# Optimization experiments

Hardware: AMD Instinct MI355X
Metric: run time of the kernel (lower is better)

## Reference

```python
import jax, jax.numpy as jnp
import numpy as np

MARGIN = 0.2
EPS = 1e-6  # torch.pairwise_distance default eps added to (x1 - x2)


def setup_inputs() -> dict:
    key = jax.random.key(0)
    k1, k2 = jax.random.split(key)
    N, D = 8192, 128
    x = jax.random.normal(k1, (N, D), dtype=jnp.float32)
    target = jax.random.randint(k2, (N,), 0, 1000)
    return {"x": x, "target": target}


def _pairwise_dist(x):
    # torch.pairwise_distance(x.unsqueeze(0), x.unsqueeze(1)):
    #   diff[i, j] = x[j] - x[i] + EPS ; dist[i, j] = ||diff[i, j]||_2
    # Expanded quadratic form avoids the [N, N, D] diff tensor:
    #   ||a - b + e||^2 = ||a||^2 + ||b||^2 - 2 a.b + 2e*sum(a - b) + D*e^2
    sq = jnp.sum(x * x, axis=1)          # [N]
    s = jnp.sum(x, axis=1)               # [N]
    dot = x @ x.T                        # [N, N]
    D = x.shape[1]
    d2 = (sq[None, :] + sq[:, None] - 2.0 * dot
          + 2.0 * EPS * (s[None, :] - s[:, None]) + D * EPS * EPS)
    return jnp.sqrt(jnp.maximum(d2, 0.0))


def reference(x, target):
    N = x.shape[0]
    dist = _pairwise_dist(x)                                 # [N, N]
    same = target[None, :] == target[:, None]                # [N, N] bool
    pos_mask = (same & ~jnp.eye(N, dtype=bool)).astype(x.dtype)
    hardest_pos = jnp.max(pos_mask * dist, axis=1, keepdims=True)  # [N, 1]
    neg_mask = (~same).astype(x.dtype)
    max_neg = jnp.max(dist, axis=1, keepdims=True)           # [N, 1]
    anchor_neg = dist + max_neg * (1.0 - neg_mask)           # push positives up
    hardest_neg = jnp.min(anchor_neg, axis=1, keepdims=True) # [N, 1]
    loss = jax.nn.relu(hardest_pos - hardest_neg + MARGIN)
    return jnp.mean(loss)
```

## Files before the change

### kernel.cpp

```cpp
#include <hip/hip_runtime.h>

#define N 8192
#define Dk 128
#define NC 1024
#define EPSC 1e-6f
#define MARGIN 0.2f

typedef __attribute__((ext_vector_type(8))) short bf16x8;
typedef __attribute__((ext_vector_type(4))) float f32x4;

__device__ __forceinline__ unsigned short f2bf(float f) {
    unsigned u = __float_as_uint(f);
    u = (u + 0x7FFFu + ((u >> 16) & 1u)) >> 16;
    return (unsigned short)u;
}

__global__ void hist_kernel(const int* __restrict__ tgt, int* __restrict__ hist) {
    int i = blockIdx.x * 256 + threadIdx.x;
    atomicAdd(&hist[tgt[i]], 1);
}

__global__ void scan_kernel(const int* __restrict__ hist, int* __restrict__ pref,
                            int* __restrict__ cursor) {
    __shared__ int tmp[NC];
    int t = threadIdx.x;
    int h = hist[t];
    tmp[t] = h;
    __syncthreads();
#pragma unroll
    for (int off = 1; off < NC; off <<= 1) {
        int v = (t >= off) ? tmp[t - off] : 0;
        __syncthreads();
        tmp[t] += v;
        __syncthreads();
    }
    int ex = tmp[t] - h;
    pref[t] = ex;
    cursor[t] = ex;
}

__global__ void scatter_kernel(const int* __restrict__ tgt, const int* __restrict__ pref,
                               const int* __restrict__ hist, int* __restrict__ cursor,
                               int* __restrict__ perm, uint2* __restrict__ band,
                               int* __restrict__ cls) {
    int i = blockIdx.x * 256 + threadIdx.x;
    int c = tgt[i];
    int pos = atomicAdd(&cursor[c], 1);
    perm[pos] = i;
    uint2 b;
    b.x = (unsigned)pref[c];
    b.y = (unsigned)(pref[c] + hist[c]);
    band[pos] = b;
    cls[pos] = c;
}

__global__ void prep_kernel(const float* __restrict__ x, const int* __restrict__ perm,
                            uint4* __restrict__ Frag, float* __restrict__ Qh,
                            float* __restrict__ P) {
    int wv = blockIdx.x * 4 + (threadIdx.x >> 6);
    int lane = threadIdx.x & 63;
    int k = wv * 4 + (lane >> 4);
    int c = lane & 15;
    int orig = perm[k];
    const float4* x4 = reinterpret_cast<const float4*>(x);
    float4 v0 = x4[orig * 32 + c * 2];
    float4 v1 = x4[orig * 32 + c * 2 + 1];
    float sq = v0.x * v0.x + v0.y * v0.y + v0.z * v0.z + v0.w * v0.w +
               v1.x * v1.x + v1.y * v1.y + v1.z * v1.z + v1.w * v1.w;
    float s = v0.x + v0.y + v0.z + v0.w + v1.x + v1.y + v1.z + v1.w;
    ushort4 lo, hi;
    lo.x = f2bf(v0.x); lo.y = f2bf(v0.y); lo.z = f2bf(v0.z); lo.w = f2bf(v0.w);
    hi.x = f2bf(v1.x); hi.y = f2bf(v1.y); hi.z = f2bf(v1.z); hi.w = f2bf(v1.w);
    uint4 pk;
    pk.x = (unsigned)lo.x | ((unsigned)lo.y << 16);
    pk.y = (unsigned)lo.z | ((unsigned)lo.w << 16);
    pk.z = (unsigned)hi.x | ((unsigned)hi.y << 16);
    pk.w = (unsigned)hi.z | ((unsigned)hi.w << 16);
    Frag[((k >> 4) * 4 + (c >> 2)) * 64 + (c & 3) * 16 + (k & 15)] = pk;
#pragma unroll
    for (int m = 1; m <= 8; m <<= 1) {
        sq += __shfl_xor(sq, m);
        s += __shfl_xor(s, m);
    }
    if (c == 0) {
        P[k] = sq - 2.0f * EPSC * s;
        Qh[k] = -0.5f * (sq + 2.0f * EPSC * s + (float)Dk * EPSC * EPSC);
    }
}

#define LOADB(Bb, Qq, t)                                                \
    do {                                                                \
        const int jt_ = jt0 + (t);                                      \
        Bb[0] = Fr[(jt_ * 4 + 0) * 64 + lane];                          \
        Bb[1] = Fr[(jt_ * 4 + 1) * 64 + lane];                          \
        Bb[2] = Fr[(jt_ * 4 + 2) * 64 + lane];                          \
        Bb[3] = Fr[(jt_ * 4 + 3) * 64 + lane];                          \
        Qq = *reinterpret_cast<const f32x4*>(&Qh[jt_ * 16 + 4 * q]);    \
    } while (0)

#define MFMA16(ACC, Bb, Qq)                                                           \
    do {                                                                              \
        _Pragma("unroll")                                                             \
        for (int ti = 0; ti < 4; ++ti) {                                              \
            ACC[ti] = __builtin_amdgcn_mfma_f32_16x16x32_bf16(Bb[0], Af[ti][0], Qq, 0, 0, 0); \
            ACC[ti] = __builtin_amdgcn_mfma_f32_16x16x32_bf16(Bb[1], Af[ti][1], ACC[ti], 0, 0, 0); \
            ACC[ti] = __builtin_amdgcn_mfma_f32_16x16x32_bf16(Bb[2], Af[ti][2], ACC[ti], 0, 0, 0); \
            ACC[ti] = __builtin_amdgcn_mfma_f32_16x16x32_bf16(Bb[3], Af[ti][3], ACC[ti], 0, 0, 0); \
        }                                                                             \
    } while (0)

#define EPILOGUE(ACC, t)                                                              \
    do {                                                                              \
        const int jc_ = (jt0 + (t)) * 16;                                             \
        if (jc_ < bHi && jc_ + 16 > bLo) {     \
            int4 cj = *reinterpret_cast<const int4*>(&cls[jc_ + 4 * q]);              \
            _Pragma("unroll")                                                         \
            for (int ti = 0; ti < 4; ++ti) {                                          \
                f32x4 v = ACC[ti];                                                    \
                int mc = myc[ti];                                                     \
                hp[ti] = fminf(hp[ti], cj.x == mc ? v[0] : INFINITY);                 \
                hp[ti] = fminf(hp[ti], cj.y == mc ? v[1] : INFINITY);                 \
                hp[ti] = fminf(hp[ti], cj.z == mc ? v[2] : INFINITY);                 \
                hp[ti] = fminf(hp[ti], cj.w == mc ? v[3] : INFINITY);                 \
                mn[ti] = fmaxf(mn[ti], cj.x == mc ? -INFINITY : v[0]);                \
                mn[ti] = fmaxf(mn[ti], cj.y == mc ? -INFINITY : v[1]);                \
                mn[ti] = fmaxf(mn[ti], cj.z == mc ? -INFINITY : v[2]);                \
                mn[ti] = fmaxf(mn[ti], cj.w == mc ? -INFINITY : v[3]);                \
            }                                                                         \
        } else {                \
            _Pragma("unroll")                                                         \
            for (int ti = 0; ti < 4; ++ti) {                                          \
                f32x4 v = ACC[ti];                                                    \
                mn[ti] = fmaxf(mn[ti], fmaxf(fmaxf(v[0], v[1]), fmaxf(v[2], v[3])));  \
            }                                                                         \
        }                                                                             \
    } while (0)

#define STEP(t, ACCc, ACCp, Bc, Qc, Bp, Qp)   \
    do {                                      \
        MFMA16(ACCc, Bc, Qc);                 \
        if ((t) + 2 < 16) LOADB(Bp, Qp, (t) + 2); \
        if ((t) > 0) EPILOGUE(ACCp, (t) - 1); \
    } while (0)

__global__ __launch_bounds__(256, 2) void main_kernel(
        const uint4* __restrict__ Frag, const float* __restrict__ Qh,
        const int* __restrict__ cls, const uint2* __restrict__ band,
        float* __restrict__ partHp, float* __restrict__ partMn) {
    const int w = threadIdx.x >> 6;
    const int lane = threadIdx.x & 63;
    const int n = lane & 15;
    const int q = lane >> 4;

    const int ig = (int)blockIdx.x >> 5;
    const int jg = (int)blockIdx.x & 31;
    const int rw = ig * 256 + 64 * w;
    const int jt0 = jg * 16;

    const bf16x8* Fr = reinterpret_cast<const bf16x8*>(Frag);

    const int bLo = (int)band[rw].x;
    const int bHi = (int)band[rw + 63].y;

    bf16x8 Af[4][4];
#pragma unroll
    for (int ti = 0; ti < 4; ++ti)
#pragma unroll
        for (int kk = 0; kk < 4; ++kk)
            Af[ti][kk] = Fr[(((rw >> 4) + ti) * 4 + kk) * 64 + lane];

    int myc[4];
#pragma unroll
    for (int ti = 0; ti < 4; ++ti) myc[ti] = cls[rw + 16 * ti + n];

    float hp[4], mn[4];
#pragma unroll
    for (int s = 0; s < 4; ++s) {
        hp[s] = INFINITY;
        mn[s] = -INFINITY;
    }

    bf16x8 B0[4], B1[4], B2[4];
    f32x4 Q0, Q1, Q2;
    f32x4 accA[4], accB[4];

    LOADB(B0, Q0, 0);
    LOADB(B1, Q1, 1);
    STEP(0, accA, accB, B0, Q0, B2, Q2);
    STEP(1, accB, accA, B1, Q1, B0, Q0);
    STEP(2, accA, accB, B2, Q2, B1, Q1);
    STEP(3, accB, accA, B0, Q0, B2, Q2);
    STEP(4, accA, accB, B1, Q1, B0, Q0);
    STEP(5, accB, accA, B2, Q2, B1, Q1);
    STEP(6, accA, accB, B0, Q0, B2, Q2);
    STEP(7, accB, accA, B1, Q1, B0, Q0);
    STEP(8, accA, accB, B2, Q2, B1, Q1);
    STEP(9, accB, accA, B0, Q0, B2, Q2);
    STEP(10, accA, accB, B1, Q1, B0, Q0);
    STEP(11, accB, accA, B2, Q2, B1, Q1);
    STEP(12, accA, accB, B0, Q0, B2, Q2);
    STEP(13, accB, accA, B1, Q1, B0, Q0);
    STEP(14, accA, accB, B2, Q2, B1, Q1);
    STEP(15, accB, accA, B0, Q0, B2, Q2);
    EPILOGUE(accB, 15);

#pragma unroll
    for (int m = 16; m <= 32; m <<= 1) {
#pragma unroll
        for (int s = 0; s < 4; ++s) {
            hp[s] = fminf(hp[s], __shfl_xor(hp[s], m));
            mn[s] = fmaxf(mn[s], __shfl_xor(mn[s], m));
        }
    }
    if (q == 0) {
#pragma unroll
        for (int ti = 0; ti < 4; ++ti) {
            int i = rw + 16 * ti + n;
            partHp[jg * N + i] = hp[ti];
            partMn[jg * N + i] = mn[ti];
        }
    }
}

__global__ void finish_kernel(const float* __restrict__ P,
                              const float* __restrict__ partHp,
                              const float* __restrict__ partMn,
                              float* __restrict__ out) {
    int i = blockIdx.x * 256 + threadIdx.x;
    float hpm = INFINITY, mnm = -INFINITY;
#pragma unroll
    for (int wg = 0; wg < 32; ++wg) {
        hpm = fminf(hpm, partHp[wg * N + i]);
        mnm = fmaxf(mnm, partMn[wg * N + i]);
    }
    float Pi = P[i];
    float hp = sqrtf(fmaxf(fmaf(-2.0f, hpm, Pi), 0.0f));
    float hn = sqrtf(fmaxf(fmaf(-2.0f, mnm, Pi), 0.0f));
    float sum = fmaxf(hp - hn + MARGIN, 0.0f) * (1.0f / (float)N);
#pragma unroll
    for (int m = 32; m >= 1; m >>= 1) sum += __shfl_xor(sum, m);
    __shared__ float ws[4];
    int lane = threadIdx.x & 63, wv = threadIdx.x >> 6;
    if (lane == 0) ws[wv] = sum;
    __syncthreads();
    if (threadIdx.x == 0) atomicAdd(out, ws[0] + ws[1] + ws[2] + ws[3]);
}

extern "C" void kernel_launch(void* const* d_in, const int* in_sizes, int n_in,
                              void* d_out, int out_size, void* d_ws, size_t ws_size,
                              hipStream_t stream) {
    const float* x = (const float*)d_in[0];
    const int* tgt = (const int*)d_in[1];
    float* out = (float*)d_out;

    char* ws = (char*)d_ws;
    size_t off = 0;
    uint4* Frag = (uint4*)(ws + off); off += (size_t)N * Dk * 2;
    float* Qh = (float*)(ws + off); off += (size_t)N * 4;
    float* P = (float*)(ws + off); off += (size_t)N * 4;
    float* partHp = (float*)(ws + off); off += (size_t)32 * N * 4;
    float* partMn = (float*)(ws + off); off += (size_t)32 * N * 4;
    uint2* band = (uint2*)(ws + off); off += (size_t)N * 8;
    int* perm = (int*)(ws + off); off += (size_t)N * 4;
    int* cls = (int*)(ws + off); off += (size_t)N * 4;
    int* hist = (int*)(ws + off); off += NC * 4;
    int* pref = (int*)(ws + off); off += NC * 4;
    int* cursor = (int*)(ws + off); off += NC * 4;

    hipMemsetAsync(hist, 0, NC * 4, stream);
    hipMemsetAsync(d_out, 0, sizeof(float), stream);
    hist_kernel<<<N / 256, 256, 0, stream>>>(tgt, hist);
    scan_kernel<<<1, NC, 0, stream>>>(hist, pref, cursor);
    scatter_kernel<<<N / 256, 256, 0, stream>>>(tgt, pref, hist, cursor, perm, band, cls);
    prep_kernel<<<N / 16, 256, 0, stream>>>(x, perm, Frag, Qh, P);
    main_kernel<<<1024, 256, 0, stream>>>(Frag, Qh, cls, band, partHp, partMn);
    finish_kernel<<<32, 256, 0, stream>>>(P, partHp, partMn, out);
}
```

Measured before the change: 102.7 us.

## Switch to 32x32x16 MFMA tiles and fuse label sort into one kernel

The main distance kernel moves from 16x16x32 bf16 MFMAs to 32x32x16 MFMAs, with a new 32-row fragment layout, per-tile packed Q and class arrays, and a two-deep double-buffered loop. Each block now covers a wider column range, so there are fewer column groups (8 instead of 32) and a smaller partial reduction in finish. The histogram, scan and scatter kernels plus both memsets are merged into one single-block shared-memory sort kernel, and a small qpack kernel is added that also zeroes the output. The aim is fewer launches and denser MFMA work per wave, at the cost of fewer blocks (512) and a larger register footprint.

Result: slower. 110.4 us (+7.5%).

```diff
diff --git a/kernel.cpp b/kernel.cpp
--- a/kernel.cpp
+++ b/kernel.cpp
@@ -7,7 +7,7 @@
 #define MARGIN 0.2f
 
 typedef __attribute__((ext_vector_type(8))) short bf16x8;
-typedef __attribute__((ext_vector_type(4))) float f32x4;
+typedef __attribute__((ext_vector_type(16))) float f32x16;
 
 __device__ __forceinline__ unsigned short f2bf(float f) {
     unsigned u = __float_as_uint(f);
@@ -15,43 +15,45 @@
     return (unsigned short)u;
 }
 
-__global__ void hist_kernel(const int* __restrict__ tgt, int* __restrict__ hist) {
-    int i = blockIdx.x * 256 + threadIdx.x;
-    atomicAdd(&hist[tgt[i]], 1);
-}
-
-__global__ void scan_kernel(const int* __restrict__ hist, int* __restrict__ pref,
-                            int* __restrict__ cursor) {
-    __shared__ int tmp[NC];
+__global__ void sort_kernel(const int* __restrict__ tgt, int* __restrict__ perm,
+                            int* __restrict__ cls, uint2* __restrict__ band) {
+    __shared__ int histS[NC], prefS[NC], curS[NC];
     int t = threadIdx.x;
-    int h = hist[t];
-    tmp[t] = h;
-    __syncthreads();
-#pragma unroll
+    histS[t] = 0;
+    __syncthreads();
+    int myt[8];
+#pragma unroll
+    for (int k = 0; k < 8; ++k) {
+        myt[k] = tgt[k * 1024 + t];
+        atomicAdd(&histS[myt[k]], 1);
+    }
+    __syncthreads();
+    int h = histS[t];
+    prefS[t] = h;
+    __syncthreads();
     for (int off = 1; off < NC; off <<= 1) {
-        int v = (t >= off) ? tmp[t - off] : 0;
+        int v = (t >= off) ? prefS[t - off] : 0;
         __syncthreads();
-        tmp[t] += v;
+        prefS[t] += v;
         __syncthreads();
     }
-    int ex = tmp[t] - h;
-    pref[t] = ex;
-    cursor[t] = ex;
-}
-
-__global__ void scatter_kernel(const int* __restrict__ tgt, const int* __restrict__ pref,
-                               const int* __restrict__ hist, int* __restrict__ cursor,
-                               int* __restrict__ perm, uint2* __restrict__ band,
-                               int* __restrict__ cls) {
-    int i = blockIdx.x * 256 + threadIdx.x;
-    int c = tgt[i];
-    int pos = atomicAdd(&cursor[c], 1);
-    perm[pos] = i;
-    uint2 b;
-    b.x = (unsigned)pref[c];
-    b.y = (unsigned)(pref[c] + hist[c]);
-    band[pos] = b;
-    cls[pos] = c;
+    int ex = prefS[t] - h;
+    __syncthreads();
+    prefS[t] = ex;
+    curS[t] = ex;
+    __syncthreads();
+#pragma unroll
+    for (int k = 0; k < 8; ++k) {
+        int i = k * 1024 + t;
+        int c = myt[k];
+        int pos = atomicAdd(&curS[c], 1);
+        perm[pos] = i;
+        cls[pos] = c;
+        uint2 b;
+        b.x = (unsigned)prefS[c];
+        b.y = (unsigned)(prefS[c] + histS[c]);
+        band[pos] = b;
+    }
 }
 
 __global__ void prep_kernel(const float* __restrict__ x, const int* __restrict__ perm,
@@ -76,7 +78,7 @@
     pk.y = (unsigned)lo.z | ((unsigned)lo.w << 16);
     pk.z = (unsigned)hi.x | ((unsigned)hi.y << 16);
     pk.w = (unsigned)hi.z | ((unsigned)hi.w << 16);
-    Frag[((k >> 4) * 4 + (c >> 2)) * 64 + (c & 3) * 16 + (k & 15)] = pk;
+    Frag[(((k >> 5) * 8) + (c >> 1)) * 64 + (c & 1) * 32 + (k & 31)] = pk;
 #pragma unroll
     for (int m = 1; m <= 8; m <<= 1) {
         sq += __shfl_xor(sq, m);
@@ -88,137 +90,113 @@
     }
 }
 
-#define LOADB(Bb, Qq, t)                                                \
-    do {                                                                \
-        const int jt_ = jt0 + (t);                                      \
-        Bb[0] = Fr[(jt_ * 4 + 0) * 64 + lane];                          \
-        Bb[1] = Fr[(jt_ * 4 + 1) * 64 + lane];                          \
-        Bb[2] = Fr[(jt_ * 4 + 2) * 64 + lane];                          \
-        Bb[3] = Fr[(jt_ * 4 + 3) * 64 + lane];                          \
-        Qq = *reinterpret_cast<const f32x4*>(&Qh[jt_ * 16 + 4 * q]);    \
+__global__ void qpack_kernel(const float* __restrict__ Qh, const int* __restrict__ cls,
+                             float4* __restrict__ Qpk, int4* __restrict__ Cpk,
+                             float* __restrict__ out) {
+    int o = blockIdx.x * 256 + threadIdx.x;
+    int base = (o >> 3) * 32 + (o & 3) * 8 + ((o >> 2) & 1) * 4;
+    float4 qv;
+    qv.x = Qh[base + 0]; qv.y = Qh[base + 1]; qv.z = Qh[base + 2]; qv.w = Qh[base + 3];
+    Qpk[o] = qv;
+    int4 cv;
+    cv.x = cls[base + 0]; cv.y = cls[base + 1]; cv.z = cls[base + 2]; cv.w = cls[base + 3];
+    Cpk[o] = cv;
+    if (o == 0) out[0] = 0.0f;
+}
+
+#define STAGE(Bx, ax, t)                                                         \
+    do {                                                                         \
+        const int jt_ = jt0 + (t);                                               \
+        _Pragma("unroll") for (int kk = 0; kk < 8; ++kk)                         \
+            Bx[kk] = Fr[(jt_ * 8 + kk) * 64 + lane];                             \
+        float4 q0_ = Qpk[jt_ * 8 + 4 * h + 0];                                   \
+        float4 q1_ = Qpk[jt_ * 8 + 4 * h + 1];                                   \
+        float4 q2_ = Qpk[jt_ * 8 + 4 * h + 2];                                   \
+        float4 q3_ = Qpk[jt_ * 8 + 4 * h + 3];                                   \
+        ax = (f32x16){q0_.x, q0_.y, q0_.z, q0_.w, q1_.x, q1_.y, q1_.z, q1_.w,    \
+                      q2_.x, q2_.y, q2_.z, q2_.w, q3_.x, q3_.y, q3_.z, q3_.w};   \
     } while (0)
 
-#define MFMA16(ACC, Bb, Qq)                                                           \
-    do {                                                                              \
-        _Pragma("unroll")                                                             \
-        for (int ti = 0; ti < 4; ++ti) {                                              \
-            ACC[ti] = __builtin_amdgcn_mfma_f32_16x16x32_bf16(Bb[0], Af[ti][0], Qq, 0, 0, 0); \
-            ACC[ti] = __builtin_amdgcn_mfma_f32_16x16x32_bf16(Bb[1], Af[ti][1], ACC[ti], 0, 0, 0); \
-            ACC[ti] = __builtin_amdgcn_mfma_f32_16x16x32_bf16(Bb[2], Af[ti][2], ACC[ti], 0, 0, 0); \
-            ACC[ti] = __builtin_amdgcn_mfma_f32_16x16x32_bf16(Bb[3], Af[ti][3], ACC[ti], 0, 0, 0); \
-        }                                                                             \
+#define MFMA8(ax, Bx)                                                            \
+    do {                                                                         \
+        _Pragma("unroll") for (int kk = 0; kk < 8; ++kk)                         \
+            ax = __builtin_amdgcn_mfma_f32_32x32x16_bf16(Bx[kk], Af[kk], ax, 0, 0, 0); \
     } while (0)
 
-#define EPILOGUE(ACC, t)                                                              \
-    do {                                                                              \
-        const int jc_ = (jt0 + (t)) * 16;                                             \
-        if (jc_ < bHi && jc_ + 16 > bLo) {     \
-            int4 cj = *reinterpret_cast<const int4*>(&cls[jc_ + 4 * q]);              \
-            _Pragma("unroll")                                                         \
-            for (int ti = 0; ti < 4; ++ti) {                                          \
-                f32x4 v = ACC[ti];                                                    \
-                int mc = myc[ti];                                                     \
-                hp[ti] = fminf(hp[ti], cj.x == mc ? v[0] : INFINITY);                 \
-                hp[ti] = fminf(hp[ti], cj.y == mc ? v[1] : INFINITY);                 \
-                hp[ti] = fminf(hp[ti], cj.z == mc ? v[2] : INFINITY);                 \
-                hp[ti] = fminf(hp[ti], cj.w == mc ? v[3] : INFINITY);                 \
-                mn[ti] = fmaxf(mn[ti], cj.x == mc ? -INFINITY : v[0]);                \
-                mn[ti] = fmaxf(mn[ti], cj.y == mc ? -INFINITY : v[1]);                \
-                mn[ti] = fmaxf(mn[ti], cj.z == mc ? -INFINITY : v[2]);                \
-                mn[ti] = fmaxf(mn[ti], cj.w == mc ? -INFINITY : v[3]);                \
-            }                                                                         \
-        } else {                \
-            _Pragma("unroll")                                                         \
-            for (int ti = 0; ti < 4; ++ti) {                                          \
-                f32x4 v = ACC[ti];                                                    \
-                mn[ti] = fmaxf(mn[ti], fmaxf(fmaxf(v[0], v[1]), fmaxf(v[2], v[3])));  \
-            }                                                                         \
-        }                                                                             \
+#define EPI(ax, t)                                                               \
+    do {                                                                         \
+        const int jt_ = jt0 + (t);                                               \
+        if (jt_ * 32 < bHi && jt_ * 32 + 32 > bLo) {  \
+            _Pragma("unroll") for (int g = 0; g < 4; ++g) {                      \
+                int4 cj = Cpk[jt_ * 8 + 4 * h + g];                              \
+                hp = fminf(hp, cj.x == myc ? ax[4 * g + 0] : INFINITY);          \
+                hp = fminf(hp, cj.y == myc ? ax[4 * g + 1] : INFINITY);          \
+                hp = fminf(hp, cj.z == myc ? ax[4 * g + 2] : INFINITY);          \
+                hp = fminf(hp, cj.w == myc ? ax[4 * g + 3] : INFINITY);          \
+                mn = fmaxf(mn, cj.x == myc ? -INFINITY : ax[4 * g + 0]);         \
+                mn = fmaxf(mn, cj.y == myc ? -INFINITY : ax[4 * g + 1]);         \
+                mn = fmaxf(mn, cj.z == myc ? -INFINITY : ax[4 * g + 2]);         \
+                mn = fmaxf(mn, cj.w == myc ? -INFINITY : ax[4 * g + 3]);         \
+            }                                                                    \
+        } else {                                                                 \
+            float m0_ = fmaxf(ax[0], ax[1]), m1_ = fmaxf(ax[2], ax[3]);          \
+            float m2_ = fmaxf(ax[4], ax[5]), m3_ = fmaxf(ax[6], ax[7]);          \
+            float m4_ = fmaxf(ax[8], ax[9]), m5_ = fmaxf(ax[10], ax[11]);        \
+            float m6_ = fmaxf(ax[12], ax[13]), m7_ = fmaxf(ax[14], ax[15]);      \
+            m0_ = fmaxf(m0_, m1_); m2_ = fmaxf(m2_, m3_);                        \
+            m4_ = fmaxf(m4_, m5_); m6_ = fmaxf(m6_, m7_);                        \
+            mn = fmaxf(mn, fmaxf(fmaxf(m0_, m2_), fmaxf(m4_, m6_)));             \
+        }                                                                        \
     } while (0)
 
-#define STEP(t, ACCc, ACCp, Bc, Qc, Bp, Qp)   \
-    do {                                      \
-        MFMA16(ACCc, Bc, Qc);                 \
-        if ((t) + 2 < 16) LOADB(Bp, Qp, (t) + 2); \
-        if ((t) > 0) EPILOGUE(ACCp, (t) - 1); \
-    } while (0)
-
 __global__ __launch_bounds__(256, 2) void main_kernel(
-        const uint4* __restrict__ Frag, const float* __restrict__ Qh,
-        const int* __restrict__ cls, const uint2* __restrict__ band,
+        const uint4* __restrict__ Frag, const float4* __restrict__ Qpk,
+        const int4* __restrict__ Cpk, const int* __restrict__ cls,
+        const uint2* __restrict__ band,
         float* __restrict__ partHp, float* __restrict__ partMn) {
+    const int lane = threadIdx.x & 63;
     const int w = threadIdx.x >> 6;
-    const int lane = threadIdx.x & 63;
-    const int n = lane & 15;
-    const int q = lane >> 4;
-
-    const int ig = (int)blockIdx.x >> 5;
-    const int jg = (int)blockIdx.x & 31;
-    const int rw = ig * 256 + 64 * w;
-    const int jt0 = jg * 16;
+    const int nn = lane & 31;
+    const int h = lane >> 5;
+
+    const int ig = (int)blockIdx.x >> 3;
+    const int jg = (int)blockIdx.x & 7;
+    const int rw = ig * 128 + 32 * w;
+    const int jt0 = jg * 32;
 
     const bf16x8* Fr = reinterpret_cast<const bf16x8*>(Frag);
 
     const int bLo = (int)band[rw].x;
-    const int bHi = (int)band[rw + 63].y;
-
-    bf16x8 Af[4][4];
-#pragma unroll
-    for (int ti = 0; ti < 4; ++ti)
-#pragma unroll
-        for (int kk = 0; kk < 4; ++kk)
-            Af[ti][kk] = Fr[(((rw >> 4) + ti) * 4 + kk) * 64 + lane];
-
-    int myc[4];
-#pragma unroll
-    for (int ti = 0; ti < 4; ++ti) myc[ti] = cls[rw + 16 * ti + n];
-
-    float hp[4], mn[4];
-#pragma unroll
-    for (int s = 0; s < 4; ++s) {
-        hp[s] = INFINITY;
-        mn[s] = -INFINITY;
-    }
-
-    bf16x8 B0[4], B1[4], B2[4];
-    f32x4 Q0, Q1, Q2;
-    f32x4 accA[4], accB[4];
-
-    LOADB(B0, Q0, 0);
-    LOADB(B1, Q1, 1);
-    STEP(0, accA, accB, B0, Q0, B2, Q2);
-    STEP(1, accB, accA, B1, Q1, B0, Q0);
-    STEP(2, accA, accB, B2, Q2, B1, Q1);
-    STEP(3, accB, accA, B0, Q0, B2, Q2);
-    STEP(4, accA, accB, B1, Q1, B0, Q0);
-    STEP(5, accB, accA, B2, Q2, B1, Q1);
-    STEP(6, accA, accB, B0, Q0, B2, Q2);
-    STEP(7, accB, accA, B1, Q1, B0, Q0);
-    STEP(8, accA, accB, B2, Q2, B1, Q1);
-    STEP(9, accB, accA, B0, Q0, B2, Q2);
-    STEP(10, accA, accB, B1, Q1, B0, Q0);
-    STEP(11, accB, accA, B2, Q2, B1, Q1);
-    STEP(12, accA, accB, B0, Q0, B2, Q2);
-    STEP(13, accB, accA, B1, Q1, B0, Q0);
-    STEP(14, accA, accB, B2, Q2, B1, Q1);
-    STEP(15, accB, accA, B0, Q0, B2, Q2);
-    EPILOGUE(accB, 15);
-
-#pragma unroll
-    for (int m = 16; m <= 32; m <<= 1) {
-#pragma unroll
-        for (int s = 0; s < 4; ++s) {
-            hp[s] = fminf(hp[s], __shfl_xor(hp[s], m));
-            mn[s] = fmaxf(mn[s], __shfl_xor(mn[s], m));
-        }
-    }
-    if (q == 0) {
-#pragma unroll
-        for (int ti = 0; ti < 4; ++ti) {
-            int i = rw + 16 * ti + n;
-            partHp[jg * N + i] = hp[ti];
-            partMn[jg * N + i] = mn[ti];
-        }
+    const int bHi = (int)band[rw + 31].y;
+    const int myc = cls[rw + nn];
+
+    bf16x8 Af[8];
+#pragma unroll
+    for (int kk = 0; kk < 8; ++kk) Af[kk] = Fr[((rw >> 5) * 8 + kk) * 64 + lane];
+
+    float hp = INFINITY;
+    float mn = -INFINITY;
+
+    bf16x8 B0[8], B1[8];
+    f32x16 a0, a1;
+
+    STAGE(B0, a0, 0);
+    STAGE(B1, a1, 1);
+#pragma unroll
+    for (int t = 0; t < 32; t += 2) {
+        MFMA8(a0, B0);
+        MFMA8(a1, B1);
+        EPI(a0, t);
+        if (t + 2 < 32) STAGE(B0, a0, t + 2);
+        EPI(a1, t + 1);
+        if (t + 3 < 32) STAGE(B1, a1, t + 3);
+    }
+
+    hp = fminf(hp, __shfl_xor(hp, 32));
+    mn = fmaxf(mn, __shfl_xor(mn, 32));
+    if (h == 0) {
+        partHp[jg * N + rw + nn] = hp;
+        partMn[jg * N + rw + nn] = mn;
     }
 }
 
@@ -229,7 +207,7 @@
     int i = blockIdx.x * 256 + threadIdx.x;
     float hpm = INFINITY, mnm = -INFINITY;
 #pragma unroll
-    for (int wg = 0; wg < 32; ++wg) {
+    for (int wg = 0; wg < 8; ++wg) {
         hpm = fminf(hpm, partHp[wg * N + i]);
         mnm = fmaxf(mnm, partMn[wg * N + i]);
     }
@@ -258,21 +236,17 @@
     uint4* Frag = (uint4*)(ws + off); off += (size_t)N * Dk * 2;
     float* Qh = (float*)(ws + off); off += (size_t)N * 4;
     float* P = (float*)(ws + off); off += (size_t)N * 4;
-    float* partHp = (float*)(ws + off); off += (size_t)32 * N * 4;
-    float* partMn = (float*)(ws + off); off += (size_t)32 * N * 4;
+    float4* Qpk = (float4*)(ws + off); off += (size_t)2048 * 16;
+    int4* Cpk = (int4*)(ws + off); off += (size_t)2048 * 16;
+    float* partHp = (float*)(ws + off); off += (size_t)8 * N * 4;
+    float* partMn = (float*)(ws + off); off += (size_t)8 * N * 4;
     uint2* band = (uint2*)(ws + off); off += (size_t)N * 8;
     int* perm = (int*)(ws + off); off += (size_t)N * 4;
     int* cls = (int*)(ws + off); off += (size_t)N * 4;
-    int* hist = (int*)(ws + off); off += NC * 4;
-    int* pref = (int*)(ws + off); off += NC * 4;
-    int* cursor = (int*)(ws + off); off += NC * 4;
-
-    hipMemsetAsync(hist, 0, NC * 4, stream);
-    hipMemsetAsync(d_out, 0, sizeof(float), stream);
-    hist_kernel<<<N / 256, 256, 0, stream>>>(tgt, hist);
-    scan_kernel<<<1, NC, 0, stream>>>(hist, pref, cursor);
-    scatter_kernel<<<N / 256, 256, 0, stream>>>(tgt, pref, hist, cursor, perm, band, cls);
+
+    sort_kernel<<<1, 1024, 0, stream>>>(tgt, perm, cls, band);
     prep_kernel<<<N / 16, 256, 0, stream>>>(x, perm, Frag, Qh, P);
-    main_kernel<<<1024, 256, 0, stream>>>(Frag, Qh, cls, band, partHp, partMn);
+    qpack_kernel<<<8, 256, 0, stream>>>(Qh, cls, Qpk, Cpk, out);
+    main_kernel<<<512, 256, 0, stream>>>(Frag, Qpk, Cpk, cls, band, partHp, partMn);
     finish_kernel<<<32, 256, 0, stream>>>(P, partHp, partMn, out);
 }
```
